# Kernel optimization log

Hardware: AMD Instinct MI355X
Metric: run time of the kernel (lower is better)

## Reference

```python
import jax, jax.numpy as jnp
import numpy as np

B, S, E, H = 4, 2048, 1024, 16
D = E // H  # head_dim = 64
SCALE = D ** -0.5
NEG_INF = -1e9


def setup_inputs() -> dict:
    key = jax.random.key(0)
    ks = jax.random.split(key, 12)
    p = 1.0 / np.sqrt(E)  # nn.Linear default init scale
    inp = {
        'query': jax.random.normal(ks[0], (B, S, E), jnp.float32),
        'key': jax.random.normal(ks[1], (B, S, E), jnp.float32),
        'value': jax.random.normal(ks[2], (B, S, E), jnp.float32),
        'mask': jnp.ones((B, S, S), jnp.int32),
        'Wq': jax.random.uniform(ks[3], (E, E), jnp.float32, -p, p),
        'bq': jax.random.uniform(ks[4], (E,), jnp.float32, -p, p),
        'Wk': jax.random.uniform(ks[5], (E, E), jnp.float32, -p, p),
        'bk': jax.random.uniform(ks[6], (E,), jnp.float32, -p, p),
        'Wv': jax.random.uniform(ks[7], (E, E), jnp.float32, -p, p),
        'bv': jax.random.uniform(ks[8], (E,), jnp.float32, -p, p),
        'Wo': jax.random.uniform(ks[9], (E, E), jnp.float32, -p, p),
        'bo': jax.random.uniform(ks[10], (E,), jnp.float32, -p, p),
    }
    return inp


def _heads(x):
    # [B, S, E] -> [B, H, S, D]
    b, s, _ = x.shape
    return x.reshape(b, s, H, D).transpose(0, 2, 1, 3)


def reference(query, key, value, mask, Wq, bq, Wk, bk, Wv, bv, Wo, bo):
    # separate QKV projections (nn.Linear: x @ W.T + b)
    q = _heads(query @ Wq.T + bq) * SCALE  # query pre-scaled as in module
    k = _heads(key @ Wk.T + bk)
    v = _heads(value @ Wv.T + bv)
    # scaled dot-product attention with explicit score matrix
    scores = jnp.einsum('bhqd,bhkd->bhqk', q, k)  # [B, H, S, S]
    m = mask[:, None, :, :]  # broadcast over heads
    scores = jnp.where(m == 0, NEG_INF, scores)
    attn = jax.nn.softmax(scores, axis=-1)
    out = jnp.einsum('bhqk,bhkd->bhqd', attn, v)  # [B, H, S, D]
    out = out.transpose(0, 2, 1, 3).reshape(query.shape[0], -1, E)
    return out @ Wo.T + bo
```

## Files before the change

### kernel.cpp

```cpp
#include <hip/hip_runtime.h>


#define B_ 4
#define S_ 2048
#define E_ 1024
#define H_ 16
#define D_ 64

typedef __attribute__((ext_vector_type(4))) float f32x4;
typedef __attribute__((ext_vector_type(8))) short short8;
typedef __attribute__((ext_vector_type(4))) short short4v;
typedef __attribute__((ext_vector_type(8))) __bf16 bf16x8;
typedef __attribute__((ext_vector_type(4))) __bf16 bf16x4;
typedef unsigned short u16;
typedef unsigned int u32;

#define MFMA16(A, Bf, C) __builtin_amdgcn_mfma_f32_16x16x32_bf16((A), (Bf), (C), 0, 0, 0)

#define FMAXB2 12.0f

__device__ __forceinline__ f32x4 mfma_pv(short4v a, short4v b, f32x4 c) {
  return __builtin_amdgcn_mfma_f32_16x16x16bf16_1k(a, b, c, 0, 0, 0);
}

__device__ __forceinline__ u16 f2bf(float f) {
  u32 u = __float_as_uint(f);
  u += 0x7FFFu + ((u >> 16) & 1u);
  return (u16)(u >> 16);
}

__device__ __forceinline__ void async16(const void* g, void* l) {
  __builtin_amdgcn_global_load_lds((const __attribute__((address_space(1))) u32*)g,
                                   (__attribute__((address_space(3))) u32*)l, 16, 0, 0);
}

__device__ __forceinline__ short4v packp(float a, float b, float c, float d) {
  bf16x4 t;
  t[0] = (__bf16)a; t[1] = (__bf16)b; t[2] = (__bf16)c; t[3] = (__bf16)d;
  return __builtin_bit_cast(short4v, t);
}

__device__ __forceinline__ float exp2fast(float x) {
  return __builtin_amdgcn_exp2f(x);
}

__global__ __launch_bounds__(256) void cvt3_kernel(const float* __restrict__ s0,
                                                   const float* __restrict__ s1,
                                                   const float* __restrict__ s2,
                                                   u16* __restrict__ d0,
                                                   u16* __restrict__ d1,
                                                   u16* __restrict__ d2, int n4) {
  int z = blockIdx.y;
  const float* src = z == 0 ? s0 : (z == 1 ? s1 : s2);
  u16* dst = z == 0 ? d0 : (z == 1 ? d1 : d2);
  int i = blockIdx.x * 256 + threadIdx.x;
  if (i >= n4) return;
  float4 v = ((const float4*)src)[i];
  short4v o;
  o[0] = (short)f2bf(v.x); o[1] = (short)f2bf(v.y);
  o[2] = (short)f2bf(v.z); o[3] = (short)f2bf(v.w);
  ((short4v*)dst)[i] = o;
}

__global__ __launch_bounds__(256) void cvt4_kernel(const float* __restrict__ s0,
                                                   const float* __restrict__ s1,
                                                   const float* __restrict__ s2,
                                                   const float* __restrict__ s3,
                                                   u16* __restrict__ d0,
                                                   u16* __restrict__ d1,
                                                   u16* __restrict__ d2,
                                                   u16* __restrict__ d3, int n4) {
  int z = blockIdx.y;
  const float* src = z == 0 ? s0 : (z == 1 ? s1 : (z == 2 ? s2 : s3));
  u16* dst = z == 0 ? d0 : (z == 1 ? d1 : (z == 2 ? d2 : d3));
  int i = blockIdx.x * 256 + threadIdx.x;
  if (i >= n4) return;
  float4 v = ((const float4*)src)[i];
  short4v o;
  o[0] = (short)f2bf(v.x); o[1] = (short)f2bf(v.y);
  o[2] = (short)f2bf(v.z); o[3] = (short)f2bf(v.w);
  ((short4v*)dst)[i] = o;
}

__global__ __launch_bounds__(64) void mask_pack_kernel(const int* __restrict__ mask,
                                                       u32* __restrict__ mbits,
                                                       int* __restrict__ rowOK) {
  int row = blockIdx.x;
  int t = threadIdx.x;
  const int4* p = (const int4*)(mask + (size_t)row * S_ + t * 32);
  u32 bits = 0;
#pragma unroll
  for (int i = 0; i < 8; ++i) {
    int4 v = p[i];
    bits |= (v.x != 0 ? 1u : 0u) << (i * 4 + 0);
    bits |= (v.y != 0 ? 1u : 0u) << (i * 4 + 1);
    bits |= (v.z != 0 ? 1u : 0u) << (i * 4 + 2);
    bits |= (v.w != 0 ? 1u : 0u) << (i * 4 + 3);
  }
  mbits[(size_t)row * 64 + t] = bits;
  unsigned long long all1 = __ballot(bits == 0xFFFFFFFFu);
  if (t == 0) rowOK[row] = (all1 == 0xFFFFFFFFFFFFFFFFull) ? 1 : 0;
}

__device__ __forceinline__ void gemm_mainloop_128(const u16* __restrict__ A,
                                                  const u16* __restrict__ W,
                                                  int m0, int n0,
                                                  u16* As, u16* Bs,
                                                  f32x4 acc[4][4], int tid) {
  int w = tid >> 6, l = tid & 63, lo = l & 15, g = l >> 4;
  int wm = w >> 1, wn = w & 1;
  int srow = w * 32 + (l >> 2);
  int scol = (l & 3) * 8;
  const u16* ga0 = A + (size_t)(m0 + srow) * E_ + scol;
  const u16* gb0 = W + (size_t)(n0 + srow) * E_ + scol;
  char* la0 = (char*)As + w * 2048;
  char* lb0 = (char*)Bs + w * 2048;

  for (int k0 = 0; k0 < E_; k0 += 32) {
    async16(ga0 + k0, la0);
    async16(ga0 + 16 * E_ + k0, la0 + 1024);
    async16(gb0 + k0, lb0);
    async16(gb0 + 16 * E_ + k0, lb0 + 1024);
    __syncthreads();
    bf16x8 af[4], bf[4];
#pragma unroll
    for (int mi = 0; mi < 4; ++mi)
      af[mi] = *(const bf16x8*)(As + (wm * 64 + mi * 16 + lo) * 32 + g * 8);
#pragma unroll
    for (int ni = 0; ni < 4; ++ni)
      bf[ni] = *(const bf16x8*)(Bs + (wn * 64 + ni * 16 + lo) * 32 + g * 8);
#pragma unroll
    for (int mi = 0; mi < 4; ++mi)
#pragma unroll
      for (int ni = 0; ni < 4; ++ni)
        acc[mi][ni] = MFMA16(af[mi], bf[ni], acc[mi][ni]);
    __syncthreads();
  }
}

__device__ __forceinline__ void gemm_swizzle(int* m0, int* n0) {
  int s = blockIdx.y * 8 + blockIdx.x;
  int L = (s & 7) * 64 + (s >> 3);
  *m0 = (L >> 3) * 128;
  *n0 = (L & 7) * 128;
}

__global__ __launch_bounds__(256) void gemm_qkv_kernel(
    const u16* __restrict__ qin, const u16* __restrict__ kin, const u16* __restrict__ vin,
    const u16* __restrict__ wq, const u16* __restrict__ wk, const u16* __restrict__ wv,
    const float* __restrict__ bq, const float* __restrict__ bk, const float* __restrict__ bv,
    u16* __restrict__ Qo, u16* __restrict__ Ko, u16* __restrict__ Vo) {
  __shared__ u16 As[128 * 32];
  __shared__ u16 Bs[128 * 32];
  int z = blockIdx.z;
  const u16* A = z == 0 ? qin : (z == 1 ? kin : vin);
  const u16* W = z == 0 ? wq : (z == 1 ? wk : wv);
  const float* bias = z == 0 ? bq : (z == 1 ? bk : bv);
  u16* O = z == 0 ? Qo : (z == 1 ? Ko : Vo);
  float scale = z == 0 ? 0.125f * 1.44269504f : 1.0f;
  int m0, n0;
  gemm_swizzle(&m0, &n0);
  f32x4 acc[4][4];
#pragma unroll
  for (int mi = 0; mi < 4; ++mi)
#pragma unroll
    for (int ni = 0; ni < 4; ++ni) acc[mi][ni] = (f32x4){0.f, 0.f, 0.f, 0.f};
  int tid = threadIdx.x;
  gemm_mainloop_128(A, W, m0, n0, As, Bs, acc, tid);
  int w = tid >> 6, l = tid & 63, lo = l & 15, g = l >> 4;
  int wm = w >> 1, wn = w & 1;
#pragma unroll
  for (int mi = 0; mi < 4; ++mi)
#pragma unroll
    for (int ni = 0; ni < 4; ++ni) {
      int n = n0 + wn * 64 + ni * 16 + lo;
      int h = n >> 6, d = n & 63;
      float bb = bias[n];
      int mbase = m0 + wm * 64 + mi * 16 + g * 4;
      int b = mbase >> 11, s = mbase & 2047;
      if (z == 2) {
        short4v ov;
#pragma unroll
        for (int j = 0; j < 4; ++j) ov[j] = (short)f2bf(acc[mi][ni][j] + bb);
        *(short4v*)(O + (((size_t)(b * H_ + h)) * D_ + d) * S_ + s) = ov;
      } else {
#pragma unroll
        for (int j = 0; j < 4; ++j) {
          float val = (acc[mi][ni][j] + bb) * scale;
          O[(((size_t)(b * H_ + h)) * S_ + (s + j)) * D_ + d] = f2bf(val);
        }
      }
    }
}

__global__ __launch_bounds__(256) void gemm_out_kernel(const u16* __restrict__ A,
                                                       const u16* __restrict__ W,
                                                       const float* __restrict__ bias,
                                                       float* __restrict__ O) {
  __shared__ u16 As[128 * 32];
  __shared__ u16 Bs[128 * 32];
  int m0, n0;
  gemm_swizzle(&m0, &n0);
  f32x4 acc[4][4];
#pragma unroll
  for (int mi = 0; mi < 4; ++mi)
#pragma unroll
    for (int ni = 0; ni < 4; ++ni) acc[mi][ni] = (f32x4){0.f, 0.f, 0.f, 0.f};
  int tid = threadIdx.x;
  gemm_mainloop_128(A, W, m0, n0, As, Bs, acc, tid);
  int w = tid >> 6, l = tid & 63, lo = l & 15, g = l >> 4;
  int wm = w >> 1, wn = w & 1;
#pragma unroll
  for (int mi = 0; mi < 4; ++mi)
#pragma unroll
    for (int ni = 0; ni < 4; ++ni) {
      int n = n0 + wn * 64 + ni * 16 + lo;
      float bb = bias[n];
#pragma unroll
      for (int j = 0; j < 4; ++j) {
        int m = m0 + wm * 64 + mi * 16 + g * 4 + j;
        O[(size_t)m * E_ + n] = acc[mi][ni][j] + bb;
      }
    }
}

__global__ __launch_bounds__(256) void attn_kernel(const u16* __restrict__ Q,
                                                   const u16* __restrict__ K,
                                                   const u16* __restrict__ VT,
                                                   u16* __restrict__ AO,
                                                   const u32* __restrict__ mbits,
                                                   const int* __restrict__ rowOK) {
  __shared__ u16 Kt0[4096], Kt1[4096];
  __shared__ u16 Vt0[4096], Vt1[4096];
  __shared__ int s_ok;

  int tid = threadIdx.x;
  int w = tid >> 6, l = tid & 63, lo = l & 15, g = l >> 4;
  int flat = blockIdx.y * gridDim.x + blockIdx.x;
  int L = (flat & 7) * 128 + (flat >> 3);
  int bh = L >> 4;
  int b = bh >> 4, h = bh & 15;
  int q0 = (L & 15) * 128;

  if (tid == 0) s_ok = 1;
  __syncthreads();
  if (tid < 128 && rowOK[b * S_ + q0 + tid] == 0) s_ok = 0;
  __syncthreads();
  const bool use_mask = (s_ok == 0);

  const u16* Qb = Q + (size_t)bh * S_ * D_;
  const u16* Kb = K + (size_t)bh * S_ * D_;
  const u16* VTb = VT + (size_t)bh * D_ * S_;

  const u16* kg[2];
  const u16* vgb[2];
  int lbase[2];
#pragma unroll
  for (int r = 0; r < 2; ++r) {
    int kb = r * 4 + w;
    int tr = kb * 8 + (l >> 3);
    int dc = (l & 7) ^ (l >> 3);
    kg[r] = Kb + (size_t)tr * D_ + dc * 8;
    vgb[r] = VTb + (size_t)tr * S_ + dc * 8;
    lbase[r] = kb * 512;
  }
#pragma unroll
  for (int r = 0; r < 2; ++r) {
    async16(kg[r], &Kt0[lbase[r]]);
    async16(vgb[r], &Vt0[lbase[r]]);
  }

  int qrow = q0 + w * 32;
  bf16x8 qf[2][2];
#pragma unroll
  for (int qi = 0; qi < 2; ++qi)
#pragma unroll
    for (int kc = 0; kc < 2; ++kc)
      qf[qi][kc] = *(const bf16x8*)(Qb + (size_t)(qrow + qi * 16 + lo) * D_ + kc * 32 + g * 8);

  f32x4 ot[4][2];
  f32x4 lacc[2];
#pragma unroll
  for (int di = 0; di < 4; ++di)
#pragma unroll
    for (int qi = 0; qi < 2; ++qi) ot[di][qi] = (f32x4){0.f, 0.f, 0.f, 0.f};
  lacc[0] = (f32x4){0.f, 0.f, 0.f, 0.f};
  lacc[1] = (f32x4){0.f, 0.f, 0.f, 0.f};
  float m_run[2] = {-__builtin_inff(), -__builtin_inff()};
  const short4v onesv = {(short)0x3F80, (short)0x3F80, (short)0x3F80, (short)0x3F80};
  const f32x4 cinit = {-FMAXB2, -FMAXB2, -FMAXB2, -FMAXB2};

  auto tile_body = [&](const u16* KtC, const u16* VtC, u16* KtN, u16* VtN, int kk) {
    __syncthreads();
    if (kk + 64 < S_) {
#pragma unroll
      for (int r = 0; r < 2; ++r) {
        async16(kg[r] + (size_t)(kk + 64) * D_, &KtN[lbase[r]]);
        async16(vgb[r] + (kk + 64), &VtN[lbase[r]]);
      }
    }
    const char* Ktc = (const char*)KtC;
    const char* Vtc = (const char*)VtC;

    short4v pb[4][2];
    if (!use_mask) {
      __builtin_amdgcn_s_setprio(1);
#pragma unroll
      for (int ks = 0; ks < 4; ++ks) {
        int row = ks * 16 + lo;
        bf16x8 a0 = *(const bf16x8*)(Ktc + row * 128 + ((g * 16) ^ ((row & 7) << 4)));
        bf16x8 a1 = *(const bf16x8*)(Ktc + row * 128 + ((64 + g * 16) ^ ((row & 7) << 4)));
        f32x4 c0 = MFMA16(a0, qf[0][0], cinit);
        c0 = MFMA16(a1, qf[0][1], c0);
        f32x4 c1 = MFMA16(a0, qf[1][0], cinit);
        c1 = MFMA16(a1, qf[1][1], c1);
        pb[ks][0] = packp(exp2fast(c0[0]), exp2fast(c0[1]), exp2fast(c0[2]),
                          exp2fast(c0[3]));
        pb[ks][1] = packp(exp2fast(c1[0]), exp2fast(c1[1]), exp2fast(c1[2]),
                          exp2fast(c1[3]));
      }
      __builtin_amdgcn_s_setprio(0);
    } else {
      float tmx[2] = {-__builtin_inff(), -__builtin_inff()};
#pragma unroll
      for (int ks = 0; ks < 4; ++ks) {
        int row = ks * 16 + lo;
        bf16x8 a0 = *(const bf16x8*)(Ktc + row * 128 + ((g * 16) ^ ((row & 7) << 4)));
        bf16x8 a1 = *(const bf16x8*)(Ktc + row * 128 + ((64 + g * 16) ^ ((row & 7) << 4)));
#pragma unroll
        for (int qi = 0; qi < 2; ++qi) {
          f32x4 c = MFMA16(a0, qf[qi][0], cinit);
          c = MFMA16(a1, qf[qi][1], c);
          int q = qrow + qi * 16 + lo;
          u32 word = mbits[((size_t)(b * S_ + q)) * 64 + ((kk + ks * 16 + g * 4) >> 5)];
#pragma unroll
          for (int j = 0; j < 4; ++j) {
            int kkk = ks * 16 + g * 4 + j;
            if (!((word >> ((kk + kkk) & 31)) & 1u)) c[j] = -1e9f;
            tmx[qi] = fmaxf(tmx[qi], c[j]);
          }
        }
      }
#pragma unroll
      for (int qi = 0; qi < 2; ++qi) {
        float t = tmx[qi];
        t = fmaxf(t, __shfl_xor(t, 16, 64));
        t = fmaxf(t, __shfl_xor(t, 32, 64));
        float mnew = fmaxf(m_run[qi], t);
        float alpha = exp2fast(m_run[qi] - mnew);
        m_run[qi] = mnew;
#pragma unroll
        for (int di = 0; di < 4; ++di) ot[di][qi] *= alpha;
        lacc[qi] *= alpha;
      }
#pragma unroll
      for (int ks = 0; ks < 4; ++ks) {
        int row = ks * 16 + lo;
        bf16x8 a0 = *(const bf16x8*)(Ktc + row * 128 + ((g * 16) ^ ((row & 7) << 4)));
        bf16x8 a1 = *(const bf16x8*)(Ktc + row * 128 + ((64 + g * 16) ^ ((row & 7) << 4)));
#pragma unroll
        for (int qi = 0; qi < 2; ++qi) {
          f32x4 c = MFMA16(a0, qf[qi][0], cinit);
          c = MFMA16(a1, qf[qi][1], c);
          int q = qrow + qi * 16 + lo;
          u32 word = mbits[((size_t)(b * S_ + q)) * 64 + ((kk + ks * 16 + g * 4) >> 5)];
          float mm = m_run[qi];
#pragma unroll
          for (int j = 0; j < 4; ++j) {
            int kkk = ks * 16 + g * 4 + j;
            if (!((word >> ((kk + kkk) & 31)) & 1u)) c[j] = -1e9f;
            c[j] = exp2fast(c[j] - mm);
          }
          pb[ks][qi] = packp(c[0], c[1], c[2], c[3]);
        }
      }
    }

#pragma unroll
    for (int ks = 0; ks < 4; ++ks)
#pragma unroll
      for (int qi = 0; qi < 2; ++qi)
        lacc[qi] = mfma_pv(onesv, pb[ks][qi], lacc[qi]);

    short4v vaA[4], vaB[4];
#define LOADVA(arr, ksv)                                                              \
  _Pragma("unroll") for (int di = 0; di < 4; ++di) {                                  \
    int r = di * 16 + lo;                                                             \
    int chunk = (ksv)*2 + (g >> 1);                                                   \
    arr[di] = *(const short4v*)(Vtc + r * 128 + (((chunk * 16) ^ ((r & 7) << 4))) +   \
                                ((g & 1) * 8));                                       \
  }
#define MFMAKS(arr, ksv)                                                              \
  _Pragma("unroll") for (int qi = 0; qi < 2; ++qi) {                                  \
    _Pragma("unroll") for (int di = 0; di < 4; ++di)                                  \
        ot[di][qi] = mfma_pv(arr[di], pb[ksv][qi], ot[di][qi]);                       \
  }
    LOADVA(vaA, 0)
    LOADVA(vaB, 1)
    __builtin_amdgcn_s_setprio(1);
    MFMAKS(vaA, 0)
    LOADVA(vaA, 2)
    MFMAKS(vaB, 1)
    LOADVA(vaB, 3)
    MFMAKS(vaA, 2)
    MFMAKS(vaB, 3)
    __builtin_amdgcn_s_setprio(0);
#undef LOADVA
#undef MFMAKS
  };

  for (int k0 = 0; k0 < S_; k0 += 128) {
    tile_body(Kt0, Vt0, Kt1, Vt1, k0);
    tile_body(Kt1, Vt1, Kt0, Vt0, k0 + 64);
  }

#pragma unroll
  for (int qi = 0; qi < 2; ++qi) {
    float inv = 1.f / lacc[qi][0];
    int q = qrow + qi * 16 + lo;
#pragma unroll
    for (int di = 0; di < 4; ++di) {
      f32x4 o = ot[di][qi] * inv;
      short4v ov = packp(o[0], o[1], o[2], o[3]);
      *(short4v*)(AO + ((size_t)(b * S_ + q)) * E_ + h * 64 + di * 16 + g * 4) = ov;
    }
  }
}

extern "C" void kernel_launch(void* const* d_in, const int* in_sizes, int n_in,
                              void* d_out, int out_size, void* d_ws, size_t ws_size,
                              hipStream_t stream) {
  const float* query = (const float*)d_in[0];
  const float* key   = (const float*)d_in[1];
  const float* value = (const float*)d_in[2];
  const int*   mask  = (const int*)d_in[3];
  const float* Wq = (const float*)d_in[4];
  const float* bq = (const float*)d_in[5];
  const float* Wk = (const float*)d_in[6];
  const float* bk = (const float*)d_in[7];
  const float* Wv = (const float*)d_in[8];
  const float* bv = (const float*)d_in[9];
  const float* Wo = (const float*)d_in[10];
  const float* bo = (const float*)d_in[11];
  float* out = (float*)d_out;

  char* ws = (char*)d_ws;
  size_t off = 0;
  auto alloc = [&](size_t bytes) -> char* {
    char* p = ws + off;
    off += (bytes + 255) & ~(size_t)255;
    return p;
  };
  const size_t ACT = (size_t)8192 * 1024 * 2;
  const size_t WMT = (size_t)1024 * 1024 * 2;
  u16* qbf = (u16*)alloc(ACT);
  u16* kbf = (u16*)alloc(ACT);
  u16* vbf = (u16*)alloc(ACT);
  u16* wqb = (u16*)alloc(WMT);
  u16* wkb = (u16*)alloc(WMT);
  u16* wvb = (u16*)alloc(WMT);
  u16* wob = (u16*)alloc(WMT);
  u16* Qd = (u16*)alloc(ACT);
  u16* Kd = (u16*)alloc(ACT);
  u16* VTd = (u16*)alloc(ACT);
  u16* AO = (u16*)alloc(ACT);
  u32* mb = (u32*)alloc((size_t)B_ * S_ * 64 * 4);
  int* rOK = (int*)alloc((size_t)B_ * S_ * 4);
  (void)in_sizes; (void)n_in; (void)out_size; (void)ws_size;

  int n4a = B_ * S_ * E_ / 4;
  int n4w = E_ * E_ / 4;
  cvt3_kernel<<<dim3((n4a + 255) / 256, 3), 256, 0, stream>>>(query, key, value, qbf, kbf,
                                                              vbf, n4a);
  cvt4_kernel<<<dim3((n4w + 255) / 256, 4), 256, 0, stream>>>(Wq, Wk, Wv, Wo, wqb, wkb, wvb,
                                                              wob, n4w);
  mask_pack_kernel<<<B_ * S_, 64, 0, stream>>>(mask, mb, rOK);
  gemm_qkv_kernel<<<dim3(8, 64, 3), 256, 0, stream>>>(
      qbf, kbf, vbf, wqb, wkb, wvb, bq, bk, bv, Qd, Kd, VTd);
  attn_kernel<<<dim3(16, 64), 256, 0, stream>>>(Qd, Kd, VTd, AO, mb, rOK);
  gemm_out_kernel<<<dim3(8, 64), 256, 0, stream>>>(AO, wob, bo, out);
}
```

Baseline: 243.8 us.

## Double GEMM K-tile with XOR-swizzled LDS and merge conversion kernels

Raises the GEMM mainloop K-step from 32 to 64, which halves the number of barrier pairs per tile, and XOR-swizzles the LDS column layout to avoid bank conflicts on the fragment reads. It also merges the activation and weight bf16 conversion kernels into one launch with seven grid slices. The merged launch sizes its grid for the activations, so many blocks in the weight slices exit early. LDS per block doubles to 32 KB, which may reduce occupancy.

```diff
diff --git a/kernel.cpp b/kernel.cpp
--- a/kernel.cpp
+++ b/kernel.cpp
@@ -44,15 +44,34 @@
   return __builtin_amdgcn_exp2f(x);
 }
 
-__global__ __launch_bounds__(256) void cvt3_kernel(const float* __restrict__ s0,
-                                                   const float* __restrict__ s1,
-                                                   const float* __restrict__ s2,
-                                                   u16* __restrict__ d0,
-                                                   u16* __restrict__ d1,
-                                                   u16* __restrict__ d2, int n4) {
+__global__ __launch_bounds__(256) void cvt7_kernel(const float* __restrict__ a0,
+                                                   const float* __restrict__ a1,
+                                                   const float* __restrict__ a2,
+                                                   const float* __restrict__ w0,
+                                                   const float* __restrict__ w1,
+                                                   const float* __restrict__ w2,
+                                                   const float* __restrict__ w3,
+                                                   u16* __restrict__ da0,
+                                                   u16* __restrict__ da1,
+                                                   u16* __restrict__ da2,
+                                                   u16* __restrict__ dw0,
+                                                   u16* __restrict__ dw1,
+                                                   u16* __restrict__ dw2,
+                                                   u16* __restrict__ dw3,
+                                                   int n4a, int n4w) {
   int z = blockIdx.y;
-  const float* src = z == 0 ? s0 : (z == 1 ? s1 : s2);
-  u16* dst = z == 0 ? d0 : (z == 1 ? d1 : d2);
+  const float* src;
+  u16* dst;
+  int n4;
+  switch (z) {
+    case 0: src = a0; dst = da0; n4 = n4a; break;
+    case 1: src = a1; dst = da1; n4 = n4a; break;
+    case 2: src = a2; dst = da2; n4 = n4a; break;
+    case 3: src = w0; dst = dw0; n4 = n4w; break;
+    case 4: src = w1; dst = dw1; n4 = n4w; break;
+    case 5: src = w2; dst = dw2; n4 = n4w; break;
+    default: src = w3; dst = dw3; n4 = n4w; break;
+  }
   int i = blockIdx.x * 256 + threadIdx.x;
   if (i >= n4) return;
   float4 v = ((const float4*)src)[i];
@@ -62,26 +81,6 @@
   ((short4v*)dst)[i] = o;
 }
 
-__global__ __launch_bounds__(256) void cvt4_kernel(const float* __restrict__ s0,
-                                                   const float* __restrict__ s1,
-                                                   const float* __restrict__ s2,
-                                                   const float* __restrict__ s3,
-                                                   u16* __restrict__ d0,
-                                                   u16* __restrict__ d1,
-                                                   u16* __restrict__ d2,
-                                                   u16* __restrict__ d3, int n4) {
-  int z = blockIdx.y;
-  const float* src = z == 0 ? s0 : (z == 1 ? s1 : (z == 2 ? s2 : s3));
-  u16* dst = z == 0 ? d0 : (z == 1 ? d1 : (z == 2 ? d2 : d3));
-  int i = blockIdx.x * 256 + threadIdx.x;
-  if (i >= n4) return;
-  float4 v = ((const float4*)src)[i];
-  short4v o;
-  o[0] = (short)f2bf(v.x); o[1] = (short)f2bf(v.y);
-  o[2] = (short)f2bf(v.z); o[3] = (short)f2bf(v.w);
-  ((short4v*)dst)[i] = o;
-}
-
 __global__ __launch_bounds__(64) void mask_pack_kernel(const int* __restrict__ mask,
                                                        u32* __restrict__ mbits,
                                                        int* __restrict__ rowOK) {
@@ -102,6 +101,13 @@
   if (t == 0) rowOK[row] = (all1 == 0xFFFFFFFFFFFFFFFFull) ? 1 : 0;
 }
 
+__device__ __forceinline__ void gemm_swizzle(int* m0, int* n0) {
+  int s = blockIdx.y * 8 + blockIdx.x;
+  int L = (s & 7) * 64 + (s >> 3);
+  *m0 = (L >> 3) * 128;
+  *n0 = (L & 7) * 128;
+}
+
 __device__ __forceinline__ void gemm_mainloop_128(const u16* __restrict__ A,
                                                   const u16* __restrict__ W,
                                                   int m0, int n0,
@@ -109,40 +115,41 @@
                                                   f32x4 acc[4][4], int tid) {
   int w = tid >> 6, l = tid & 63, lo = l & 15, g = l >> 4;
   int wm = w >> 1, wn = w & 1;
-  int srow = w * 32 + (l >> 2);
-  int scol = (l & 3) * 8;
+  int srow = w * 32 + (l >> 3);
+  int scol = ((l & 7) ^ (l >> 3)) * 8;
   const u16* ga0 = A + (size_t)(m0 + srow) * E_ + scol;
   const u16* gb0 = W + (size_t)(n0 + srow) * E_ + scol;
-  char* la0 = (char*)As + w * 2048;
-  char* lb0 = (char*)Bs + w * 2048;
-
-  for (int k0 = 0; k0 < E_; k0 += 32) {
-    async16(ga0 + k0, la0);
-    async16(ga0 + 16 * E_ + k0, la0 + 1024);
-    async16(gb0 + k0, lb0);
-    async16(gb0 + 16 * E_ + k0, lb0 + 1024);
+  char* la0 = (char*)As + w * 4096;
+  char* lb0 = (char*)Bs + w * 4096;
+
+  for (int k0 = 0; k0 < E_; k0 += 64) {
+#pragma unroll
+    for (int i = 0; i < 4; ++i) {
+      async16(ga0 + (size_t)i * 8 * E_ + k0, la0 + i * 1024);
+      async16(gb0 + (size_t)i * 8 * E_ + k0, lb0 + i * 1024);
+    }
     __syncthreads();
-    bf16x8 af[4], bf[4];
-#pragma unroll
-    for (int mi = 0; mi < 4; ++mi)
-      af[mi] = *(const bf16x8*)(As + (wm * 64 + mi * 16 + lo) * 32 + g * 8);
-#pragma unroll
-    for (int ni = 0; ni < 4; ++ni)
-      bf[ni] = *(const bf16x8*)(Bs + (wn * 64 + ni * 16 + lo) * 32 + g * 8);
-#pragma unroll
-    for (int mi = 0; mi < 4; ++mi)
-#pragma unroll
-      for (int ni = 0; ni < 4; ++ni)
-        acc[mi][ni] = MFMA16(af[mi], bf[ni], acc[mi][ni]);
+#pragma unroll
+    for (int kh = 0; kh < 2; ++kh) {
+      bf16x8 af[4], bf[4];
+#pragma unroll
+      for (int mi = 0; mi < 4; ++mi) {
+        int r = wm * 64 + mi * 16 + lo;
+        af[mi] = *(const bf16x8*)((char*)As + r * 128 + (((kh * 4 + g) ^ (r & 7)) * 16));
+      }
+#pragma unroll
+      for (int ni = 0; ni < 4; ++ni) {
+        int r = wn * 64 + ni * 16 + lo;
+        bf[ni] = *(const bf16x8*)((char*)Bs + r * 128 + (((kh * 4 + g) ^ (r & 7)) * 16));
+      }
+#pragma unroll
+      for (int mi = 0; mi < 4; ++mi)
+#pragma unroll
+        for (int ni = 0; ni < 4; ++ni)
+          acc[mi][ni] = MFMA16(af[mi], bf[ni], acc[mi][ni]);
+    }
     __syncthreads();
   }
-}
-
-__device__ __forceinline__ void gemm_swizzle(int* m0, int* n0) {
-  int s = blockIdx.y * 8 + blockIdx.x;
-  int L = (s & 7) * 64 + (s >> 3);
-  *m0 = (L >> 3) * 128;
-  *n0 = (L & 7) * 128;
 }
 
 __global__ __launch_bounds__(256) void gemm_qkv_kernel(
@@ -150,8 +157,8 @@
     const u16* __restrict__ wq, const u16* __restrict__ wk, const u16* __restrict__ wv,
     const float* __restrict__ bq, const float* __restrict__ bk, const float* __restrict__ bv,
     u16* __restrict__ Qo, u16* __restrict__ Ko, u16* __restrict__ Vo) {
-  __shared__ u16 As[128 * 32];
-  __shared__ u16 Bs[128 * 32];
+  __shared__ u16 As[128 * 64];
+  __shared__ u16 Bs[128 * 64];
   int z = blockIdx.z;
   const u16* A = z == 0 ? qin : (z == 1 ? kin : vin);
   const u16* W = z == 0 ? wq : (z == 1 ? wk : wv);
@@ -197,8 +204,8 @@
                                                        const u16* __restrict__ W,
                                                        const float* __restrict__ bias,
                                                        float* __restrict__ O) {
-  __shared__ u16 As[128 * 32];
-  __shared__ u16 Bs[128 * 32];
+  __shared__ u16 As[128 * 64];
+  __shared__ u16 Bs[128 * 64];
   int m0, n0;
   gemm_swizzle(&m0, &n0);
   f32x4 acc[4][4];
@@ -470,10 +477,8 @@
 
   int n4a = B_ * S_ * E_ / 4;
   int n4w = E_ * E_ / 4;
-  cvt3_kernel<<<dim3((n4a + 255) / 256, 3), 256, 0, stream>>>(query, key, value, qbf, kbf,
-                                                              vbf, n4a);
-  cvt4_kernel<<<dim3((n4w + 255) / 256, 4), 256, 0, stream>>>(Wq, Wk, Wv, Wo, wqb, wkb, wvb,
-                                                              wob, n4w);
+  cvt7_kernel<<<dim3((n4a + 255) / 256, 7), 256, 0, stream>>>(
+      query, key, value, Wq, Wk, Wv, Wo, qbf, kbf, vbf, wqb, wkb, wvb, wob, n4a, n4w);
   mask_pack_kernel<<<B_ * S_, 64, 0, stream>>>(mask, mb, rOK);
   gemm_qkv_kernel<<<dim3(8, 64, 3), 256, 0, stream>>>(
       qbf, kbf, vbf, wqb, wkb, wvb, bq, bk, bv, Qd, Kd, VTd);
```

After: 234.7 us. 3.7% less time.
